# Kernel optimization log

Hardware: AMD Instinct MI355X
Metric: run time of the kernel (lower is better)

## Reference

```python
import jax, jax.numpy as jnp
import numpy as np

B, C_IN, C_OUT, H, W = 128, 64, 64, 56, 56
NUM_EXPERTS = 8
N_ROUTED = NUM_EXPERTS - 1


def setup_inputs() -> dict:
    key = jax.random.key(0)
    ks = jax.random.split(key, 7)
    x = jax.random.normal(ks[0], (B, C_IN, H, W), dtype=jnp.float32)
    weights = jax.random.uniform(ks[1], (B,), dtype=jnp.float32)
    indices = jax.random.randint(ks[2], (B,), 0, N_ROUTED, dtype=jnp.int32)
    # shared expert: 1x1 conv == per-pixel linear, weight [out, in], bias [out]
    s = 1.0 / np.sqrt(C_IN)
    W_shared = jax.random.uniform(ks[3], (C_OUT, C_IN), minval=-s, maxval=s, dtype=jnp.float32)
    b_shared = jax.random.uniform(ks[4], (C_OUT,), minval=-s, maxval=s, dtype=jnp.float32)
    # routed experts stacked: [E, out, in] and [E, out]
    W_routed = jax.random.uniform(ks[5], (N_ROUTED, C_OUT, C_IN), minval=-s, maxval=s, dtype=jnp.float32)
    b_routed = jax.random.uniform(ks[6], (N_ROUTED, C_OUT), minval=-s, maxval=s, dtype=jnp.float32)
    return {"x": x, "weights": weights, "indices": indices,
            "W_shared": W_shared, "b_shared": b_shared,
            "W_routed": W_routed, "b_routed": b_routed}


def reference(x, weights, indices, W_shared, b_shared, W_routed, b_routed):
    # Shared expert (1x1 conv): [B,C_in,H,W] -> [B,C_out,H,W]
    shared = jnp.einsum('oi,bihw->bohw', W_shared, x) + b_shared[None, :, None, None]
    # Routed: each sample b uses expert indices[b]; gather per-sample expert params
    W_sel = W_routed[indices]           # [B, out, in]
    b_sel = b_routed[indices]           # [B, out]
    routed = jnp.einsum('boi,bihw->bohw', W_sel, x) + b_sel[:, :, None, None]
    routed = routed * weights[:, None, None, None]
    return shared + routed
```

## Files before the change

kernel.cpp:

```cpp
#include <hip/hip_runtime.h>


typedef __bf16 bf16x8 __attribute__((ext_vector_type(8)));
typedef float  f32x16 __attribute__((ext_vector_type(16)));

#define HW     3136
#define CIN    64
#define COUT   64
#define NTILES 98
#define NGRP   13

__global__ __launch_bounds__(256, 4) void moe_mfma(
    const float* __restrict__ x,
    const float* __restrict__ weights,
    const int*   __restrict__ indices,
    const float* __restrict__ W_shared,
    const float* __restrict__ b_shared,
    const float* __restrict__ W_routed,
    const float* __restrict__ b_routed,
    float* __restrict__ out)
{
    const int bs   = blockIdx.y;
    const int wave = threadIdx.x >> 6;
    const int lane = threadIdx.x & 63;
    const int l5   = lane >> 5;
    const int l31  = lane & 31;

    const float wb = weights[bs];
    const int   e  = indices[bs];
    const int   ob = (wave >> 1) * 32;

    int tile0 = blockIdx.x * 8;
    if (tile0 > NTILES - 8) tile0 = NTILES - 8;
    const int px0 = (tile0 + (wave & 1) * 4) * 32;

    bf16x8 afrag[4];
    {
        const float* Ws = W_shared + (size_t)(ob + l31) * CIN + 8 * l5;
        const float* Wr = W_routed + ((size_t)e * COUT + ob + l31) * CIN + 8 * l5;
        #pragma unroll
        for (int ks = 0; ks < 4; ++ks) {
            float4 s0 = *(const float4*)(Ws + 16 * ks);
            float4 s1 = *(const float4*)(Ws + 16 * ks + 4);
            float4 r0 = *(const float4*)(Wr + 16 * ks);
            float4 r1 = *(const float4*)(Wr + 16 * ks + 4);
            float t[8];
            t[0] = s0.x + wb * r0.x;  t[1] = s0.y + wb * r0.y;
            t[2] = s0.z + wb * r0.z;  t[3] = s0.w + wb * r0.w;
            t[4] = s1.x + wb * r1.x;  t[5] = s1.y + wb * r1.y;
            t[6] = s1.z + wb * r1.z;  t[7] = s1.w + wb * r1.w;
            #pragma unroll
            for (int j = 0; j < 8; ++j) afrag[ks][j] = (__bf16)t[j];
        }
    }

    f32x16 biasv;
    #pragma unroll
    for (int g = 0; g < 4; ++g) {
        const int o4 = ob + 8 * g + 4 * l5;
        float4 s = *(const float4*)(b_shared + o4);
        float4 r = *(const float4*)(b_routed + e * COUT + o4);
        biasv[4 * g + 0] = s.x + wb * r.x;
        biasv[4 * g + 1] = s.y + wb * r.y;
        biasv[4 * g + 2] = s.z + wb * r.z;
        biasv[4 * g + 3] = s.w + wb * r.w;
    }

    const float* __restrict__ xs = x   + (size_t)bs * CIN  * HW;
    float*       __restrict__ os = out + (size_t)bs * COUT * HW;

    #pragma unroll 1
    for (int t = 0; t < 4; ++t) {
        const int px = px0 + t * 32 + l31;
        f32x16 acc = biasv;
        #pragma unroll
        for (int ks = 0; ks < 4; ++ks) {
            const float* xp = xs + (size_t)(16 * ks + 8 * l5) * HW + px;
            float xv[8];
            #pragma unroll
            for (int j = 0; j < 8; ++j) xv[j] = xp[(size_t)j * HW];
            bf16x8 bfr;
            #pragma unroll
            for (int j = 0; j < 8; ++j) bfr[j] = (__bf16)xv[j];
            acc = __builtin_amdgcn_mfma_f32_32x32x16_bf16(afrag[ks], bfr, acc, 0, 0, 0);
        }
        #pragma unroll
        for (int r = 0; r < 16; ++r) {
            const int row = ob + (r & 3) + 8 * (r >> 2) + 4 * l5;
            os[(size_t)row * HW + px] = acc[r];
        }
    }
}

extern "C" void kernel_launch(void* const* d_in, const int* in_sizes, int n_in,
                              void* d_out, int out_size, void* d_ws, size_t ws_size,
                              hipStream_t stream) {
    const float* x        = (const float*)d_in[0];
    const float* weights  = (const float*)d_in[1];
    const int*   indices  = (const int*)  d_in[2];
    const float* W_shared = (const float*)d_in[3];
    const float* b_shared = (const float*)d_in[4];
    const float* W_routed = (const float*)d_in[5];
    const float* b_routed = (const float*)d_in[6];
    float* out = (float*)d_out;

    moe_mfma<<<dim3(NGRP, 128), 256, 0, stream>>>(
        x, weights, indices, W_shared, b_shared, W_routed, b_routed, out);
}
```

Baseline: 44.93 us.

## Stage input pixel tile in LDS via direct global-to-LDS loads

Each block now loads a 64-channel by 128-pixel tile of x once into shared memory using global_load_lds, then all four waves read their B fragments from LDS. Before this, each wave read x from global memory itself, and the two output-channel halves fetched the same pixels twice. The tile shrinks from 256 to 128 pixels per block, and the grid grows to 25 blocks per sample. This adds 32KB of LDS per block, which may limit occupancy, and a barrier that keeps the load from overlapping with compute.

```diff
diff --git a/kernel.cpp b/kernel.cpp
--- a/kernel.cpp
+++ b/kernel.cpp
@@ -1,14 +1,22 @@
 #include <hip/hip_runtime.h>
+#include <stdint.h>
 
 
 typedef __bf16 bf16x8 __attribute__((ext_vector_type(8)));
 typedef float  f32x16 __attribute__((ext_vector_type(16)));
 
-#define HW     3136
-#define CIN    64
-#define COUT   64
-#define NTILES 98
-#define NGRP   13
+#define HW    3136
+#define CIN   64
+#define COUT  64
+#define PXB   128
+#define NPXB  25
+
+__device__ __forceinline__ void g2lds16(const float* g, float* lds_base) {
+    __builtin_amdgcn_global_load_lds(
+        (const __attribute__((address_space(1))) void*)g,
+        (__attribute__((address_space(3))) void*)lds_base,
+        16, 0, 0);
+}
 
 __global__ __launch_bounds__(256, 4) void moe_mfma(
     const float* __restrict__ x,
@@ -20,7 +28,12 @@
     const float* __restrict__ b_routed,
     float* __restrict__ out)
 {
-    const int bs   = blockIdx.y;
+    __shared__ float xl[CIN * PXB];
+
+    const int bs = blockIdx.y;
+    int px0 = blockIdx.x * PXB;
+    if (px0 > HW - PXB) px0 = HW - PXB;
+
     const int wave = threadIdx.x >> 6;
     const int lane = threadIdx.x & 63;
     const int l5   = lane >> 5;
@@ -28,12 +41,17 @@
 
     const float wb = weights[bs];
     const int   e  = indices[bs];
-    const int   ob = (wave >> 1) * 32;
 
-    int tile0 = blockIdx.x * 8;
-    if (tile0 > NTILES - 8) tile0 = NTILES - 8;
-    const int px0 = (tile0 + (wave & 1) * 4) * 32;
+    const float* __restrict__ xs = x + (size_t)bs * CIN * HW;
 
+    #pragma unroll
+    for (int i = 0; i < 8; ++i) {
+        const int row = 16 * wave + 2 * i;
+        g2lds16(xs + (size_t)(row + l5) * HW + px0 + 4 * l31,
+                xl + row * PXB);
+    }
+
+    const int ob = (wave >> 1) * 32;
     bf16x8 afrag[4];
     {
         const float* Ws = W_shared + (size_t)(ob + l31) * CIN + 8 * l5;
@@ -44,16 +62,16 @@
             float4 s1 = *(const float4*)(Ws + 16 * ks + 4);
             float4 r0 = *(const float4*)(Wr + 16 * ks);
             float4 r1 = *(const float4*)(Wr + 16 * ks + 4);
-            float t[8];
-            t[0] = s0.x + wb * r0.x;  t[1] = s0.y + wb * r0.y;
-            t[2] = s0.z + wb * r0.z;  t[3] = s0.w + wb * r0.w;
-            t[4] = s1.x + wb * r1.x;  t[5] = s1.y + wb * r1.y;
-            t[6] = s1.z + wb * r1.z;  t[7] = s1.w + wb * r1.w;
-            #pragma unroll
-            for (int j = 0; j < 8; ++j) afrag[ks][j] = (__bf16)t[j];
+            afrag[ks][0] = (__bf16)(s0.x + wb * r0.x);
+            afrag[ks][1] = (__bf16)(s0.y + wb * r0.y);
+            afrag[ks][2] = (__bf16)(s0.z + wb * r0.z);
+            afrag[ks][3] = (__bf16)(s0.w + wb * r0.w);
+            afrag[ks][4] = (__bf16)(s1.x + wb * r1.x);
+            afrag[ks][5] = (__bf16)(s1.y + wb * r1.y);
+            afrag[ks][6] = (__bf16)(s1.z + wb * r1.z);
+            afrag[ks][7] = (__bf16)(s1.w + wb * r1.w);
         }
     }
-
     f32x16 biasv;
     #pragma unroll
     for (int g = 0; g < 4; ++g) {
@@ -66,28 +84,27 @@
         biasv[4 * g + 3] = s.w + wb * r.w;
     }
 
-    const float* __restrict__ xs = x   + (size_t)bs * CIN  * HW;
-    float*       __restrict__ os = out + (size_t)bs * COUT * HW;
+    __syncthreads();
 
-    #pragma unroll 1
-    for (int t = 0; t < 4; ++t) {
-        const int px = px0 + t * 32 + l31;
+    const int pxh = (wave & 1) * 64;
+    float* __restrict__ os = out + (size_t)bs * COUT * HW + px0;
+
+    #pragma unroll
+    for (int t = 0; t < 2; ++t) {
+        const int pxl = pxh + 32 * t + l31;
         f32x16 acc = biasv;
         #pragma unroll
         for (int ks = 0; ks < 4; ++ks) {
-            const float* xp = xs + (size_t)(16 * ks + 8 * l5) * HW + px;
-            float xv[8];
-            #pragma unroll
-            for (int j = 0; j < 8; ++j) xv[j] = xp[(size_t)j * HW];
             bf16x8 bfr;
             #pragma unroll
-            for (int j = 0; j < 8; ++j) bfr[j] = (__bf16)xv[j];
+            for (int j = 0; j < 8; ++j)
+                bfr[j] = (__bf16)xl[(16 * ks + 8 * l5 + j) * PXB + pxl];
             acc = __builtin_amdgcn_mfma_f32_32x32x16_bf16(afrag[ks], bfr, acc, 0, 0, 0);
         }
         #pragma unroll
         for (int r = 0; r < 16; ++r) {
             const int row = ob + (r & 3) + 8 * (r >> 2) + 4 * l5;
-            os[(size_t)row * HW + px] = acc[r];
+            os[(size_t)row * HW + pxl] = acc[r];
         }
     }
 }
@@ -104,6 +121,6 @@
     const float* b_routed = (const float*)d_in[6];
     float* out = (float*)d_out;
 
-    moe_mfma<<<dim3(NGRP, 128), 256, 0, stream>>>(
+    moe_mfma<<<dim3(NPXB, 128), 256, 0, stream>>>(
         x, weights, indices, W_shared, b_shared, W_routed, b_routed, out);
 }
```

Measured after the change: 44.96 us. Within noise of the previous version (+0.1%).
